# Kernel optimization log

Hardware: AMD Instinct MI355X
Metric: run time of the kernel (lower is better)

The kernel has to match this reference:

```python
import jax, jax.numpy as jnp
import numpy as np

# Routing structure from the torch module
GT0 = [[0,1,0,0,1,0],[0,1,0,0,0,1],[0,0,1,0,1,0],[0,0,1,0,0,1],[0,0,0,1,1,0],[0,0,0,1,0,1]]
NCLS = 6
K = 1  # top-k

def _expert_pairs():
    # For class i, expert index m = 1+(j-1)*5+(k-1) maps to atom1[j-1] -> atom2[k-1].
    pairs = []
    for i in range(NCLS):
        p = [(j - 1, k - 1) for j in range(1, 6) for k in range(1, 6)
             if j != k and GT0[i][j] == 1 and GT0[i][k] == 1]
        pairs.append(p)
    return pairs

PAIRS = _expert_pairs()  # each class has exactly 2 (atom1, atom2) pairs

B, P, D, H = 64, 256, 768, 3072

def setup_inputs() -> dict:
    key = jax.random.key(0)
    ks = jax.random.split(key, 8)
    s = 0.02
    x = jax.random.normal(ks[0], (B, NCLS + P, D), dtype=jnp.float32)
    mids = jax.random.randint(ks[1], (B,), 0, 6)
    moe0_W1 = jax.random.normal(ks[2], (D, H), dtype=jnp.float32) * s
    moe0_b1 = jnp.zeros((H,), jnp.float32)
    moe0_W2 = jax.random.normal(ks[3], (H, D), dtype=jnp.float32) * s
    moe0_b2 = jnp.zeros((D,), jnp.float32)
    A1_W = jax.random.normal(ks[4], (5, D, H), dtype=jnp.float32) * s  # atom1 linears
    A1_b = jnp.zeros((5, H), jnp.float32)
    A2_W = jax.random.normal(ks[5], (5, H, D), dtype=jnp.float32) * s  # atom2 linears
    A2_b = jnp.zeros((5, D), jnp.float32)
    G_W = jax.random.normal(ks[6], (NCLS, D, 2), dtype=jnp.float32) * s  # per-class gates (2 experts each, no bias)
    return {"x": x, "moe0_W1": moe0_W1, "moe0_b1": moe0_b1, "moe0_W2": moe0_W2,
            "moe0_b2": moe0_b2, "A1_W": A1_W, "A1_b": A1_b, "A2_W": A2_W,
            "A2_b": A2_b, "G_W": G_W, "mids": mids}

def _gelu(t):
    return jax.nn.gelu(t, approximate=False)  # torch nn.GELU default = erf

def reference(x, moe0_W1, moe0_b1, moe0_W2, moe0_b2, A1_W, A1_b, A2_W, A2_b, G_W, mids):
    cls_tokens = x[:, :NCLS]          # [B, 6, D]
    patch_tokens = x[:, NCLS:]        # [B, P, D]
    patch_out = _gelu(patch_tokens @ moe0_W1 + moe0_b1) @ moe0_W2 + moe0_b2  # [B, P, D]
    cls_outs = []
    for i in range(NCLS):
        tok = cls_tokens[:, i]        # [B, D]
        eouts = [ _gelu(tok @ A1_W[a] + A1_b[a]) @ A2_W[c] + A2_b[c] for (a, c) in PAIRS[i] ]
        out = jnp.stack(eouts, axis=-1)                 # [B, D, E=2]
        gate = jax.nn.softmax(tok @ G_W[i], axis=-1)    # [B, E]
        # top-k masking (k=1 < E=2): keep gates strictly above the (k+1)-th largest
        thr = jnp.sort(gate, axis=-1)[..., -(K + 1)]    # [B]
        mask = (gate > thr[..., None]).astype(gate.dtype)
        g = gate * mask
        g = g / jnp.clip(jnp.sum(g, axis=-1, keepdims=True), 1e-6)
        cls_outs.append(jnp.sum(out * g[:, None, :], axis=-1))  # [B, D]
    cls_out = jnp.stack(cls_outs, axis=1)               # [B, 6, D]
    return jnp.concatenate([cls_out, patch_out], axis=1)  # [B, 6+P, D]
```

## Files before the change

### kernel.cpp

```cpp
#include <hip/hip_runtime.h>
#include <hip/hip_bf16.h>

#define DD 768
#define HH 3072
#define BB 64
#define TT 262

typedef __bf16 bf16x8 __attribute__((ext_vector_type(8)));
typedef float f32x4 __attribute__((ext_vector_type(4)));
typedef unsigned short u16;
typedef unsigned int u32;

__device__ __constant__ int A_FIRST[12]  = {0,3, 0,4, 1,3, 1,4, 2,3, 2,4};
__device__ __constant__ int A_SECOND[12] = {3,0, 4,0, 3,1, 4,1, 3,2, 4,2};

__device__ __forceinline__ float gelu_f(float x) {
  float n2t = x * fmaf(x * x, -0.0713548163f, -1.5957691216f);
  return x * __builtin_amdgcn_rcpf(1.0f + __expf(n2t));
}

__device__ __forceinline__ u16 f2bf(float x) {
  u32 u = __builtin_bit_cast(u32, x);
  return (u16)((u + 0x7fffu + ((u >> 16) & 1u)) >> 16);
}

__device__ __forceinline__ void load_lds16(const void* g, void* l) {
  __builtin_amdgcn_global_load_lds(
      (const __attribute__((address_space(1))) void*)g,
      (__attribute__((address_space(3))) void*)l,
      16, 0, 0);
}

#define VMCNT(n) asm volatile("s_waitcnt vmcnt(" #n ")")
#define BAR() __builtin_amdgcn_s_barrier()

__global__ __launch_bounds__(256)
void preproc(const float* __restrict__ x,
             const float* __restrict__ W1, const float* __restrict__ A1W,
             const float* __restrict__ W2, const float* __restrict__ A2W,
             const float* __restrict__ GW,
             __hip_bfloat16* __restrict__ xb,
             __hip_bfloat16* __restrict__ W1t, __hip_bfloat16* __restrict__ A1t,
             __hip_bfloat16* __restrict__ W2t, __hip_bfloat16* __restrict__ A2t,
             int* __restrict__ sel) {
  __shared__ __hip_bfloat16 tile[32][33];
  const int bx = blockIdx.x;
  const int tid = threadIdx.x;
  if (bx < 12576) {
    int i = bx * 256 + tid;
    float4 v = ((const float4*)x)[i];
    union { u16 s[4]; uint2 d; } pk;
    pk.s[0] = f2bf(v.x); pk.s[1] = f2bf(v.y); pk.s[2] = f2bf(v.z); pk.s[3] = f2bf(v.w);
    *(uint2*)((u16*)xb + (size_t)i * 4) = pk.d;
  } else if (bx < 40224) {
    int R, C;
    const float* ip;
    __hip_bfloat16* op;
    int t;
    if (bx < 26400) {
      t = bx - 12576; R = DD; C = HH;
      int z = t / 2304; t %= 2304;
      ip = z ? (A1W + (size_t)(z - 1) * DD * HH) : W1;
      op = z ? (A1t + (size_t)(z - 1) * DD * HH) : W1t;
    } else {
      t = bx - 26400; R = HH; C = DD;
      int z = t / 2304; t %= 2304;
      ip = z ? (A2W + (size_t)(z - 1) * DD * HH) : W2;
      op = z ? (A2t + (size_t)(z - 1) * DD * HH) : W2t;
    }
    int ctiles = C >> 5;
    int c0 = (t % ctiles) * 32, r0 = (t / ctiles) * 32;
    int tx = tid & 31, ty = tid >> 5;
#pragma unroll
    for (int s = 0; s < 4; ++s) {
      int rr = ty * 4 + s;
      tile[rr][tx] = __float2bfloat16(ip[(size_t)(r0 + rr) * C + c0 + tx]);
    }
    __syncthreads();
#pragma unroll
    for (int s = 0; s < 4; ++s) {
      int cc = ty * 4 + s;
      op[(size_t)(c0 + cc) * R + r0 + tx] = tile[tx][cc];
    }
  } else {
    int unit = (bx - 40224) * 4 + (tid >> 6);
    int lane = tid & 63;
    int b = unit & 63, i = unit >> 6;
    const float* tok = x + (size_t)(b * TT + i) * DD;
    const float* g = GW + (size_t)i * DD * 2;
    float p0 = 0.f, p1 = 0.f;
    for (int k = lane; k < DD; k += 64) {
      float tv = tok[k];
      p0 += tv * g[k * 2 + 0];
      p1 += tv * g[k * 2 + 1];
    }
#pragma unroll
    for (int o = 32; o; o >>= 1) { p0 += __shfl_xor(p0, o); p1 += __shfl_xor(p1, o); }
    if (lane == 0) sel[i * 64 + b] = (p0 > p1) ? 0 : ((p1 > p0) ? 1 : 2);
  }
}

template <int MH, int KS>
__device__ __forceinline__ void rd_a(bf16x8 (&af)[4], const char* ab, int a_rd0) {
#pragma unroll
  for (int ii = 0; ii < 4; ++ii)
    af[ii] = *(const bf16x8*)(ab + MH * 16384 + ii * 2048 + (a_rd0 ^ (KS << 6)));
}
template <int KS>
__device__ __forceinline__ void rd_b(bf16x8 (&bf)[4], const char* bb, int b_rd0) {
#pragma unroll
  for (int j = 0; j < 4; ++j)
    bf[j] = *(const bf16x8*)(bb + (j >> 1) * 16384 + (j & 1) * 2048 + (b_rd0 ^ (KS << 6)));
}
template <int MH>
__device__ __forceinline__ void mma16(f32x4 (&acc)[8][4], const bf16x8 (&af)[4], const bf16x8 (&bf)[4]) {
  __builtin_amdgcn_s_setprio(1);
#pragma unroll
  for (int ii = 0; ii < 4; ++ii)
#pragma unroll
    for (int j = 0; j < 4; ++j)
      acc[MH * 4 + ii][j] =
          __builtin_amdgcn_mfma_f32_16x16x32_bf16(bf[j], af[ii], acc[MH * 4 + ii][j], 0, 0, 0);
  __builtin_amdgcn_s_setprio(0);
}

template <int MODE>
__device__ __forceinline__
void gemm_big(char* __restrict__ smem, int bx,
              const __hip_bfloat16* __restrict__ A,
              const __hip_bfloat16* __restrict__ Bw,
              const float* __restrict__ bias,
              void* __restrict__ Out) {
  constexpr int KDIM = (MODE == 0) ? DD : HH;
  constexpr int KT = KDIM / 64;
  constexpr int KB = KDIM * 2;

  char* As = smem;
  char* Bs = smem + 65536;

  const int tid = threadIdx.x;
  const int lane = tid & 63;
  const int q = lane >> 4;
  const int r = lane & 15;
  const int wave = tid >> 6;
  const int wave_m = wave >> 2;
  const int wave_n = wave & 3;

  int m0, n0;
  if constexpr (MODE == 0) {
    int chunk = bx / 192, local = bx % 192;
    m0 = (chunk * 16 + local % 16) * 256;
    n0 = (local / 16) * 256;
  } else {
    m0 = (bx % 64) * 256;
    n0 = (bx / 64) * 256;
  }

  const int trow = tid >> 3;
  const int sw = ((tid & 7) ^ (trow & 7)) << 4;
  size_t a_row;
  if constexpr (MODE == 0) a_row = (size_t)((m0 >> 8) * TT + 6 + trow);
  else                     a_row = (size_t)(m0 + trow);
  const char* gA = (const char*)A + a_row * KB + sw;
  const char* gB = (const char*)Bw + (size_t)(n0 + trow) * KB + sw;
  const int ldsb = (tid & ~63) * 16;

#define STAGE_A(h, kt, bsel) do { \
    load_lds16(gA + (size_t)((h) * 128) * KB + (kt) * 128,      As + ((bsel) << 15) + (h) * 16384 + ldsb); \
    load_lds16(gA + (size_t)((h) * 128 + 64) * KB + (kt) * 128, As + ((bsel) << 15) + (h) * 16384 + 8192 + ldsb); \
  } while (0)
#define STAGE_B(h, kt, bsel) do { \
    load_lds16(gB + (size_t)((h) * 128) * KB + (kt) * 128,      Bs + ((bsel) << 15) + (h) * 16384 + ldsb); \
    load_lds16(gB + (size_t)((h) * 128 + 64) * KB + (kt) * 128, Bs + ((bsel) << 15) + (h) * 16384 + 8192 + ldsb); \
  } while (0)

  const int a_rd0 = (wave_m * 64 + r) * 128 + ((q ^ (r & 7)) << 4);
  const int b_rd0 = (wave_n * 32 + r) * 128 + ((q ^ (r & 7)) << 4);

  f32x4 acc[8][4];
#pragma unroll
  for (int i = 0; i < 8; ++i)
#pragma unroll
    for (int j = 0; j < 4; ++j) acc[i][j] = (f32x4){0.f, 0.f, 0.f, 0.f};
  bf16x8 af[4], bf0[4], bf1[4];

  STAGE_A(0, 0, 0); STAGE_B(0, 0, 0); STAGE_B(1, 0, 0); STAGE_A(1, 0, 0);
  VMCNT(2);
  BAR();

  for (int t = 0; t < KT - 1; ++t) {
    const int bsel = t & 1, nsel = bsel ^ 1;
    const char* ab = As + (bsel << 15);
    const char* bb = Bs + (bsel << 15);
    rd_a<0, 0>(af, ab, a_rd0);
    rd_b<0>(bf0, bb, b_rd0);
    STAGE_A(0, t + 1, nsel);
    BAR();
    mma16<0>(acc, af, bf0);
    BAR();
    rd_a<0, 1>(af, ab, a_rd0);
    rd_b<1>(bf1, bb, b_rd0);
    STAGE_B(0, t + 1, nsel);
    BAR();
    mma16<0>(acc, af, bf1);
    VMCNT(4);
    BAR();
    rd_a<1, 0>(af, ab, a_rd0);
    STAGE_B(1, t + 1, nsel);
    BAR();
    mma16<1>(acc, af, bf0);
    BAR();
    rd_a<1, 1>(af, ab, a_rd0);
    STAGE_A(1, t + 1, nsel);
    BAR();
    mma16<1>(acc, af, bf1);
    VMCNT(2);
    BAR();
  }
  {
    const char* ab = As + (((KT - 1) & 1) << 15);
    const char* bb = Bs + (((KT - 1) & 1) << 15);
    rd_a<0, 0>(af, ab, a_rd0);
    rd_b<0>(bf0, bb, b_rd0);
    BAR(); mma16<0>(acc, af, bf0); BAR();
    rd_a<0, 1>(af, ab, a_rd0);
    rd_b<1>(bf1, bb, b_rd0);
    BAR(); mma16<0>(acc, af, bf1);
    VMCNT(0);
    BAR();
    rd_a<1, 0>(af, ab, a_rd0);
    BAR(); mma16<1>(acc, af, bf0); BAR();
    rd_a<1, 1>(af, ab, a_rd0);
    BAR(); mma16<1>(acc, af, bf1);
  }
#undef STAGE_A
#undef STAGE_B

#pragma unroll
  for (int i = 0; i < 8; ++i) {
    const int m_g = m0 + (i >> 2) * 128 + wave_m * 64 + (i & 3) * 16 + r;
#pragma unroll
    for (int j = 0; j < 4; ++j) {
      const int n_g = n0 + (j >> 1) * 128 + wave_n * 32 + (j & 1) * 16 + q * 4;
      f32x4 v = acc[i][j];
      v += *(const f32x4*)(bias + n_g);
      if constexpr (MODE == 0) {
        union { u16 s[4]; uint2 d; } pk;
#pragma unroll
        for (int rg = 0; rg < 4; ++rg) pk.s[rg] = f2bf(gelu_f(v[rg]));
        *(uint2*)((u16*)Out + (size_t)m_g * HH + n_g) = pk.d;
      } else {
        const int b = m_g >> 8, p = m_g & 255;
        *(f32x4*)((float*)Out + (size_t)(b * TT + 6 + p) * DD + n_g) = v;
      }
    }
  }
}

template <int MODE>
__device__ __forceinline__
void gemm_cls(char* __restrict__ smem, int bx,
              const __hip_bfloat16* __restrict__ A,
              const __hip_bfloat16* __restrict__ Bw,
              const float* __restrict__ bias,
              void* __restrict__ Out, const int* __restrict__ sel) {
  constexpr int KDIM = (MODE == 2) ? DD : HH;
  constexpr int KT = KDIM / 64;
  char* As = smem;
  char* Bs = smem + 8192;

  const int tid = threadIdx.x;
  const int lane = tid & 63;
  const int q = lane >> 4;
  const int r = lane & 15;
  const int wave = tid >> 6;
  const int wave_m = wave >> 2;
  const int wave_n = wave & 3;

  int n0, combo, e;
  if constexpr (MODE == 2) { n0 = (bx % 24) * 128; combo = bx / 24; e = A_FIRST[combo]; }
  else                     { n0 = (bx % 6) * 128;  combo = bx / 6;  e = A_SECOND[combo]; }
  const int cls_i = combo >> 1;
  const __hip_bfloat16* Bp = Bw + (size_t)e * DD * HH;
  const float* biasp = bias + e * ((MODE == 2) ? HH : DD);

  const int trow = tid >> 3;
  const int sw = ((tid & 7) ^ (trow & 7)) << 4;
  const char* gA = (const char*)A +
      ((MODE == 2) ? (size_t)(trow * TT + cls_i) * (DD * 2)
                   : (size_t)(combo * 64 + trow) * (HH * 2)) + sw;
  const char* gB = (const char*)Bp + (size_t)(n0 + trow) * (KDIM * 2) + sw;
  const int ldsb = (tid & ~63) * 16;
  const int sa = (q ^ (r & 7)) << 4;

  f32x4 acc[2][2];
  acc[0][0] = acc[0][1] = acc[1][0] = acc[1][1] = (f32x4){0.f, 0.f, 0.f, 0.f};

  for (int t = 0; t < KT; ++t) {
    load_lds16(gA + t * 128, As + ldsb);
    load_lds16(gB + t * 128, Bs + ldsb);
    load_lds16(gB + (size_t)64 * (KDIM * 2) + t * 128, Bs + 8192 + ldsb);
    __syncthreads();
#pragma unroll
    for (int ks = 0; ks < 2; ++ks) {
      bf16x8 a0 = *(const bf16x8*)(As + (wave_m * 32 + r) * 128 + (sa ^ (ks << 6)));
      bf16x8 a1 = *(const bf16x8*)(As + (wave_m * 32 + 16 + r) * 128 + (sa ^ (ks << 6)));
      bf16x8 b0 = *(const bf16x8*)(Bs + (wave_n * 32 + r) * 128 + (sa ^ (ks << 6)));
      bf16x8 b1 = *(const bf16x8*)(Bs + (wave_n * 32 + 16 + r) * 128 + (sa ^ (ks << 6)));
      acc[0][0] = __builtin_amdgcn_mfma_f32_16x16x32_bf16(b0, a0, acc[0][0], 0, 0, 0);
      acc[0][1] = __builtin_amdgcn_mfma_f32_16x16x32_bf16(b1, a0, acc[0][1], 0, 0, 0);
      acc[1][0] = __builtin_amdgcn_mfma_f32_16x16x32_bf16(b0, a1, acc[1][0], 0, 0, 0);
      acc[1][1] = __builtin_amdgcn_mfma_f32_16x16x32_bf16(b1, a1, acc[1][1], 0, 0, 0);
    }
    __syncthreads();
  }

#pragma unroll
  for (int i = 0; i < 2; ++i) {
    const int m_g = wave_m * 32 + i * 16 + r;
#pragma unroll
    for (int j = 0; j < 2; ++j) {
      const int n_g = n0 + wave_n * 32 + j * 16 + q * 4;
      f32x4 v = acc[i][j];
      v += *(const f32x4*)(biasp + n_g);
      if constexpr (MODE == 2) {
        union { u16 s[4]; uint2 d; } pk;
#pragma unroll
        for (int rg = 0; rg < 4; ++rg) pk.s[rg] = f2bf(gelu_f(v[rg]));
        *(uint2*)((u16*)Out + (size_t)(combo * 64 + m_g) * HH + n_g) = pk.d;
      } else {
        const int s = sel[cls_i * 64 + m_g];
        const int jj = combo & 1;
        float* dst = (float*)Out + (size_t)(m_g * TT + cls_i) * DD + n_g;
        if (s == jj)                    *(f32x4*)dst = v;
        else if (jj == 0 && s == 2)     *(f32x4*)dst = (f32x4){0.f, 0.f, 0.f, 0.f};
      }
    }
  }
}

__global__ __launch_bounds__(512, 2)
void mega1(const __hip_bfloat16* __restrict__ xb, const __hip_bfloat16* __restrict__ W1t,
           const float* __restrict__ b1, __hip_bfloat16* __restrict__ hid,
           const __hip_bfloat16* __restrict__ A1t, const float* __restrict__ A1b,
           __hip_bfloat16* __restrict__ hcls) {
  __shared__ __align__(16) char smem[131072];
  int bx = blockIdx.x;
  if (bx < 768) gemm_big<0>(smem, bx, xb, W1t, b1, hid);
  else          gemm_cls<2>(smem, bx - 768, xb, A1t, A1b, hcls, nullptr);
}

__global__ __launch_bounds__(512, 2)
void mega2(const __hip_bfloat16* __restrict__ hid, const __hip_bfloat16* __restrict__ W2t,
           const float* __restrict__ b2, float* __restrict__ out,
           const __hip_bfloat16* __restrict__ hcls, const __hip_bfloat16* __restrict__ A2t,
           const float* __restrict__ A2b, const int* __restrict__ sel) {
  __shared__ __align__(16) char smem[131072];
  int bx = blockIdx.x;
  if (bx < 192) gemm_big<1>(smem, bx, hid, W2t, b2, out);
  else          gemm_cls<3>(smem, bx - 192, hcls, A2t, A2b, out, sel);
}

extern "C" void kernel_launch(void* const* d_in, const int* in_sizes, int n_in,
                              void* d_out, int out_size, void* d_ws, size_t ws_size,
                              hipStream_t stream) {
  const float* x   = (const float*)d_in[0];
  const float* W1  = (const float*)d_in[1];
  const float* b1  = (const float*)d_in[2];
  const float* W2  = (const float*)d_in[3];
  const float* b2  = (const float*)d_in[4];
  const float* A1W = (const float*)d_in[5];
  const float* A1b = (const float*)d_in[6];
  const float* A2W = (const float*)d_in[7];
  const float* A2b = (const float*)d_in[8];
  const float* GW  = (const float*)d_in[9];
  float* out = (float*)d_out;

  char* ws = (char*)d_ws;
  __hip_bfloat16* xb   = (__hip_bfloat16*)(ws + 0);
  __hip_bfloat16* W1t  = (__hip_bfloat16*)(ws + 25755648);
  __hip_bfloat16* W2t  = (__hip_bfloat16*)(ws + 30474240);
  __hip_bfloat16* A1t  = (__hip_bfloat16*)(ws + 35192832);
  __hip_bfloat16* A2t  = (__hip_bfloat16*)(ws + 58785792);
  __hip_bfloat16* hcls = (__hip_bfloat16*)(ws + 82378752);
  int* sel             = (int*)(ws + 87097344);
  __hip_bfloat16* hid  = (__hip_bfloat16*)(ws + 87099136);

  preproc<<<40320, 256, 0, stream>>>(x, W1, A1W, W2, A2W, GW, xb, W1t, A1t, W2t, A2t, sel);
  mega1<<<1056, 512, 0, stream>>>(xb, W1t, b1, hid, A1t, A1b, hcls);
  mega2<<<264, 512, 0, stream>>>(hid, W2t, b2, out, hcls, A2t, A2b, sel);
}
```

Baseline: 398.6 us.

## Split LDS into named half-tile arrays and unroll GEMM K-loop by two

The single 128KB shared buffer is replaced by eight separately named 16KB arrays, so the compiler can see that the LDS regions are disjoint and schedule reads and async loads more freely. The big GEMM main loop is unrolled two K-tiles per iteration, with the stage buffers swapped statically and the vmcnt waits retuned to the new issue order. The prologue now prefetches more of the next tile. The cls GEMM is adapted to the split B halves. Risks are a longer code body and possible mis-ordering if the new wait counts are wrong.

```diff
diff --git a/kernel.cpp b/kernel.cpp
--- a/kernel.cpp
+++ b/kernel.cpp
@@ -31,7 +31,7 @@
       16, 0, 0);
 }
 
-#define VMCNT(n) asm volatile("s_waitcnt vmcnt(" #n ")")
+#define VMCNT(n) asm volatile("s_waitcnt vmcnt(" #n ")" ::: "memory")
 #define BAR() __builtin_amdgcn_s_barrier()
 
 __global__ __launch_bounds__(256)
@@ -100,18 +100,24 @@
   }
 }
 
-template <int MH, int KS>
-__device__ __forceinline__ void rd_a(bf16x8 (&af)[4], const char* ab, int a_rd0) {
+__device__ __forceinline__ void rd_a4(bf16x8 (&af)[4], const char (&arr)[16384], int base) {
 #pragma unroll
   for (int ii = 0; ii < 4; ++ii)
-    af[ii] = *(const bf16x8*)(ab + MH * 16384 + ii * 2048 + (a_rd0 ^ (KS << 6)));
-}
-template <int KS>
-__device__ __forceinline__ void rd_b(bf16x8 (&bf)[4], const char* bb, int b_rd0) {
-#pragma unroll
-  for (int j = 0; j < 4; ++j)
-    bf[j] = *(const bf16x8*)(bb + (j >> 1) * 16384 + (j & 1) * 2048 + (b_rd0 ^ (KS << 6)));
-}
+    af[ii] = *(const bf16x8*)(&arr[base + ii * 2048]);
+}
+__device__ __forceinline__ void rd_b4(bf16x8 (&bf)[4], const char (&L)[16384],
+                                      const char (&H)[16384], int base) {
+#pragma unroll
+  for (int j = 0; j < 2; ++j) {
+    bf[j]     = *(const bf16x8*)(&L[base + j * 2048]);
+    bf[2 + j] = *(const bf16x8*)(&H[base + j * 2048]);
+  }
+}
+__device__ __forceinline__ void st2(const char* g, size_t rs, char (&arr)[16384], int ldsb) {
+  load_lds16(g,      &arr[ldsb]);
+  load_lds16(g + rs, &arr[8192 + ldsb]);
+}
+
 template <int MH>
 __device__ __forceinline__ void mma16(f32x4 (&acc)[8][4], const bf16x8 (&af)[4], const bf16x8 (&bf)[4]) {
   __builtin_amdgcn_s_setprio(1);
@@ -126,25 +132,22 @@
 
 template <int MODE>
 __device__ __forceinline__
-void gemm_big(char* __restrict__ smem, int bx,
-              const __hip_bfloat16* __restrict__ A,
-              const __hip_bfloat16* __restrict__ Bw,
-              const float* __restrict__ bias,
-              void* __restrict__ Out) {
+void gemm_big(int bx,
+              char (&A0s0)[16384], char (&A1s0)[16384], char (&B0s0)[16384], char (&B1s0)[16384],
+              char (&A0s1)[16384], char (&A1s1)[16384], char (&B0s1)[16384], char (&B1s1)[16384],
+              const __hip_bfloat16* __restrict__ A, const __hip_bfloat16* __restrict__ Bw,
+              const float* __restrict__ bias, void* __restrict__ Out) {
   constexpr int KDIM = (MODE == 0) ? DD : HH;
   constexpr int KT = KDIM / 64;
-  constexpr int KB = KDIM * 2;
-
-  char* As = smem;
-  char* Bs = smem + 65536;
+  constexpr int ITER = KT / 2;
+  constexpr size_t KB = (size_t)KDIM * 2;
+  constexpr size_t R64 = 64 * KB, R128 = 128 * KB;
 
   const int tid = threadIdx.x;
   const int lane = tid & 63;
-  const int q = lane >> 4;
-  const int r = lane & 15;
+  const int q = lane >> 4, r = lane & 15;
   const int wave = tid >> 6;
-  const int wave_m = wave >> 2;
-  const int wave_n = wave & 3;
+  const int wave_m = wave >> 2, wave_n = wave & 3;
 
   int m0, n0;
   if constexpr (MODE == 0) {
@@ -165,15 +168,6 @@
   const char* gB = (const char*)Bw + (size_t)(n0 + trow) * KB + sw;
   const int ldsb = (tid & ~63) * 16;
 
-#define STAGE_A(h, kt, bsel) do { \
-    load_lds16(gA + (size_t)((h) * 128) * KB + (kt) * 128,      As + ((bsel) << 15) + (h) * 16384 + ldsb); \
-    load_lds16(gA + (size_t)((h) * 128 + 64) * KB + (kt) * 128, As + ((bsel) << 15) + (h) * 16384 + 8192 + ldsb); \
-  } while (0)
-#define STAGE_B(h, kt, bsel) do { \
-    load_lds16(gB + (size_t)((h) * 128) * KB + (kt) * 128,      Bs + ((bsel) << 15) + (h) * 16384 + ldsb); \
-    load_lds16(gB + (size_t)((h) * 128 + 64) * KB + (kt) * 128, Bs + ((bsel) << 15) + (h) * 16384 + 8192 + ldsb); \
-  } while (0)
-
   const int a_rd0 = (wave_m * 64 + r) * 128 + ((q ^ (r & 7)) << 4);
   const int b_rd0 = (wave_n * 32 + r) * 128 + ((q ^ (r & 7)) << 4);
 
@@ -184,57 +178,69 @@
     for (int j = 0; j < 4; ++j) acc[i][j] = (f32x4){0.f, 0.f, 0.f, 0.f};
   bf16x8 af[4], bf0[4], bf1[4];
 
-  STAGE_A(0, 0, 0); STAGE_B(0, 0, 0); STAGE_B(1, 0, 0); STAGE_A(1, 0, 0);
-  VMCNT(2);
+  st2(gA,          R64, A0s0, ldsb);
+  st2(gB,          R64, B0s0, ldsb);
+  st2(gB + R128,   R64, B1s0, ldsb);
+  st2(gA + R128,   R64, A1s0, ldsb);
+  st2(gA + 128,    R64, A0s1, ldsb);
+  st2(gB + 128,    R64, B0s1, ldsb);
+  VMCNT(6);
   BAR();
 
-  for (int t = 0; t < KT - 1; ++t) {
-    const int bsel = t & 1, nsel = bsel ^ 1;
-    const char* ab = As + (bsel << 15);
-    const char* bb = Bs + (bsel << 15);
-    rd_a<0, 0>(af, ab, a_rd0);
-    rd_b<0>(bf0, bb, b_rd0);
-    STAGE_A(0, t + 1, nsel);
-    BAR();
-    mma16<0>(acc, af, bf0);
-    BAR();
-    rd_a<0, 1>(af, ab, a_rd0);
-    rd_b<1>(bf1, bb, b_rd0);
-    STAGE_B(0, t + 1, nsel);
-    BAR();
-    mma16<0>(acc, af, bf1);
-    VMCNT(4);
-    BAR();
-    rd_a<1, 0>(af, ab, a_rd0);
-    STAGE_B(1, t + 1, nsel);
-    BAR();
-    mma16<1>(acc, af, bf0);
-    BAR();
-    rd_a<1, 1>(af, ab, a_rd0);
-    STAGE_A(1, t + 1, nsel);
-    BAR();
-    mma16<1>(acc, af, bf1);
-    VMCNT(2);
-    BAR();
-  }
-  {
-    const char* ab = As + (((KT - 1) & 1) << 15);
-    const char* bb = Bs + (((KT - 1) & 1) << 15);
-    rd_a<0, 0>(af, ab, a_rd0);
-    rd_b<0>(bf0, bb, b_rd0);
+  for (int i = 0; i < ITER - 1; ++i) {
+    rd_a4(af, A0s0, a_rd0);
+    rd_b4(bf0, B0s0, B1s0, b_rd0);
+    st2(gB + R128 + 128, R64, B1s1, ldsb);
     BAR(); mma16<0>(acc, af, bf0); BAR();
-    rd_a<0, 1>(af, ab, a_rd0);
-    rd_b<1>(bf1, bb, b_rd0);
-    BAR(); mma16<0>(acc, af, bf1);
-    VMCNT(0);
-    BAR();
-    rd_a<1, 0>(af, ab, a_rd0);
+    rd_a4(af, A0s0, a_rd0 ^ 64);
+    rd_b4(bf1, B0s0, B1s0, b_rd0 ^ 64);
+    st2(gA + R128 + 128, R64, A1s1, ldsb);
+    BAR(); mma16<0>(acc, af, bf1); VMCNT(8); BAR();
+    rd_a4(af, A1s0, a_rd0);
+    st2(gA + 256, R64, A0s0, ldsb);
     BAR(); mma16<1>(acc, af, bf0); BAR();
-    rd_a<1, 1>(af, ab, a_rd0);
-    BAR(); mma16<1>(acc, af, bf1);
-  }
-#undef STAGE_A
-#undef STAGE_B
+    rd_a4(af, A1s0, a_rd0 ^ 64);
+    st2(gB + 256, R64, B0s0, ldsb);
+    BAR(); mma16<1>(acc, af, bf1); VMCNT(6); BAR();
+    rd_a4(af, A0s1, a_rd0);
+    rd_b4(bf0, B0s1, B1s1, b_rd0);
+    st2(gB + R128 + 256, R64, B1s0, ldsb);
+    BAR(); mma16<0>(acc, af, bf0); BAR();
+    rd_a4(af, A0s1, a_rd0 ^ 64);
+    rd_b4(bf1, B0s1, B1s1, b_rd0 ^ 64);
+    st2(gA + R128 + 256, R64, A1s0, ldsb);
+    BAR(); mma16<0>(acc, af, bf1); VMCNT(8); BAR();
+    rd_a4(af, A1s1, a_rd0);
+    st2(gA + 384, R64, A0s1, ldsb);
+    BAR(); mma16<1>(acc, af, bf0); BAR();
+    rd_a4(af, A1s1, a_rd0 ^ 64);
+    st2(gB + 384, R64, B0s1, ldsb);
+    BAR(); mma16<1>(acc, af, bf1); VMCNT(6); BAR();
+    gA += 256; gB += 256;
+  }
+
+  rd_a4(af, A0s0, a_rd0);
+  rd_b4(bf0, B0s0, B1s0, b_rd0);
+  st2(gB + R128 + 128, R64, B1s1, ldsb);
+  BAR(); mma16<0>(acc, af, bf0); BAR();
+  rd_a4(af, A0s0, a_rd0 ^ 64);
+  rd_b4(bf1, B0s0, B1s0, b_rd0 ^ 64);
+  st2(gA + R128 + 128, R64, A1s1, ldsb);
+  BAR(); mma16<0>(acc, af, bf1); VMCNT(8); BAR();
+  rd_a4(af, A1s0, a_rd0);
+  BAR(); mma16<1>(acc, af, bf0); BAR();
+  rd_a4(af, A1s0, a_rd0 ^ 64);
+  BAR(); mma16<1>(acc, af, bf1); VMCNT(2); BAR();
+  rd_a4(af, A0s1, a_rd0);
+  rd_b4(bf0, B0s1, B1s1, b_rd0);
+  BAR(); mma16<0>(acc, af, bf0); BAR();
+  rd_a4(af, A0s1, a_rd0 ^ 64);
+  rd_b4(bf1, B0s1, B1s1, b_rd0 ^ 64);
+  BAR(); mma16<0>(acc, af, bf1); VMCNT(0); BAR();
+  rd_a4(af, A1s1, a_rd0);
+  BAR(); mma16<1>(acc, af, bf0); BAR();
+  rd_a4(af, A1s1, a_rd0 ^ 64);
+  BAR(); mma16<1>(acc, af, bf1);
 
 #pragma unroll
   for (int i = 0; i < 8; ++i) {
@@ -259,23 +265,17 @@
 
 template <int MODE>
 __device__ __forceinline__
-void gemm_cls(char* __restrict__ smem, int bx,
-              const __hip_bfloat16* __restrict__ A,
-              const __hip_bfloat16* __restrict__ Bw,
-              const float* __restrict__ bias,
-              void* __restrict__ Out, const int* __restrict__ sel) {
+void gemm_cls(int bx, char (&Asp)[16384], char (&BsL)[16384], char (&BsH)[16384],
+              const __hip_bfloat16* __restrict__ A, const __hip_bfloat16* __restrict__ Bw,
+              const float* __restrict__ bias, void* __restrict__ Out, const int* __restrict__ sel) {
   constexpr int KDIM = (MODE == 2) ? DD : HH;
   constexpr int KT = KDIM / 64;
-  char* As = smem;
-  char* Bs = smem + 8192;
 
   const int tid = threadIdx.x;
   const int lane = tid & 63;
-  const int q = lane >> 4;
-  const int r = lane & 15;
+  const int q = lane >> 4, r = lane & 15;
   const int wave = tid >> 6;
-  const int wave_m = wave >> 2;
-  const int wave_n = wave & 3;
+  const int wave_m = wave >> 2, wave_n = wave & 3;
 
   int n0, combo, e;
   if constexpr (MODE == 2) { n0 = (bx % 24) * 128; combo = bx / 24; e = A_FIRST[combo]; }
@@ -296,17 +296,20 @@
   f32x4 acc[2][2];
   acc[0][0] = acc[0][1] = acc[1][0] = acc[1][1] = (f32x4){0.f, 0.f, 0.f, 0.f};
 
+  const char* bb = (wave_n < 2) ? &BsL[0] : &BsH[0];
+  const int brow = (wave_n & 1) * 32;
+
   for (int t = 0; t < KT; ++t) {
-    load_lds16(gA + t * 128, As + ldsb);
-    load_lds16(gB + t * 128, Bs + ldsb);
-    load_lds16(gB + (size_t)64 * (KDIM * 2) + t * 128, Bs + 8192 + ldsb);
+    load_lds16(gA + t * 128, &Asp[ldsb]);
+    load_lds16(gB + t * 128, &BsL[ldsb]);
+    load_lds16(gB + (size_t)64 * (KDIM * 2) + t * 128, &BsH[ldsb]);
     __syncthreads();
 #pragma unroll
     for (int ks = 0; ks < 2; ++ks) {
-      bf16x8 a0 = *(const bf16x8*)(As + (wave_m * 32 + r) * 128 + (sa ^ (ks << 6)));
-      bf16x8 a1 = *(const bf16x8*)(As + (wave_m * 32 + 16 + r) * 128 + (sa ^ (ks << 6)));
-      bf16x8 b0 = *(const bf16x8*)(Bs + (wave_n * 32 + r) * 128 + (sa ^ (ks << 6)));
-      bf16x8 b1 = *(const bf16x8*)(Bs + (wave_n * 32 + 16 + r) * 128 + (sa ^ (ks << 6)));
+      bf16x8 a0 = *(const bf16x8*)(&Asp[(wave_m * 32 + r) * 128 + (sa ^ (ks << 6))]);
+      bf16x8 a1 = *(const bf16x8*)(&Asp[(wave_m * 32 + 16 + r) * 128 + (sa ^ (ks << 6))]);
+      bf16x8 b0 = *(const bf16x8*)(bb + (brow + r) * 128 + (sa ^ (ks << 6)));
+      bf16x8 b1 = *(const bf16x8*)(bb + (brow + 16 + r) * 128 + (sa ^ (ks << 6)));
       acc[0][0] = __builtin_amdgcn_mfma_f32_16x16x32_bf16(b0, a0, acc[0][0], 0, 0, 0);
       acc[0][1] = __builtin_amdgcn_mfma_f32_16x16x32_bf16(b1, a0, acc[0][1], 0, 0, 0);
       acc[1][0] = __builtin_amdgcn_mfma_f32_16x16x32_bf16(b0, a1, acc[1][0], 0, 0, 0);
@@ -344,10 +347,11 @@
            const float* __restrict__ b1, __hip_bfloat16* __restrict__ hid,
            const __hip_bfloat16* __restrict__ A1t, const float* __restrict__ A1b,
            __hip_bfloat16* __restrict__ hcls) {
-  __shared__ __align__(16) char smem[131072];
+  __shared__ __align__(16) char A0s0[16384], A1s0[16384], B0s0[16384], B1s0[16384],
+                                A0s1[16384], A1s1[16384], B0s1[16384], B1s1[16384];
   int bx = blockIdx.x;
-  if (bx < 768) gemm_big<0>(smem, bx, xb, W1t, b1, hid);
-  else          gemm_cls<2>(smem, bx - 768, xb, A1t, A1b, hcls, nullptr);
+  if (bx < 768) gemm_big<0>(bx, A0s0, A1s0, B0s0, B1s0, A0s1, A1s1, B0s1, B1s1, xb, W1t, b1, hid);
+  else          gemm_cls<2>(bx - 768, A0s0, B0s0, B1s0, xb, A1t, A1b, hcls, nullptr);
 }
 
 __global__ __launch_bounds__(512, 2)
@@ -355,10 +359,11 @@
            const float* __restrict__ b2, float* __restrict__ out,
            const __hip_bfloat16* __restrict__ hcls, const __hip_bfloat16* __restrict__ A2t,
            const float* __restrict__ A2b, const int* __restrict__ sel) {
-  __shared__ __align__(16) char smem[131072];
+  __shared__ __align__(16) char A0s0[16384], A1s0[16384], B0s0[16384], B1s0[16384],
+                                A0s1[16384], A1s1[16384], B0s1[16384], B1s1[16384];
   int bx = blockIdx.x;
-  if (bx < 192) gemm_big<1>(smem, bx, hid, W2t, b2, out);
-  else          gemm_cls<3>(smem, bx - 192, hcls, A2t, A2b, out, sel);
+  if (bx < 192) gemm_big<1>(bx, A0s0, A1s0, B0s0, B1s0, A0s1, A1s1, B0s1, B1s1, hid, W2t, b2, out);
+  else          gemm_cls<3>(bx - 192, A0s0, B0s0, B1s0, hcls, A2t, A2b, out, sel);
 }
 
 extern "C" void kernel_launch(void* const* d_in, const int* in_sizes, int n_in,
```

New measurement: 419.4 us. +5.2%, slower.

## Unroll big GEMM main loop by two k-tiles with deeper prefetch and inline-asm LDS reads

Applied to the files above, without the earlier changes.

Rewrites the large-GEMM main loop to process two k-tiles per iteration. Global-to-LDS staging is issued further ahead, with six quarter-tiles in flight at the prologue and vmcnt waits adjusted to match. LDS fragment reads now go through inline-asm ds_read_b128 with immediate offsets and explicit lgkmcnt waits plus sched barriers, meant to cut address arithmetic and give tighter control over MFMA/load interleaving. In exchange, manual waitcnt handling is fragile, and the sched barriers may block compiler scheduling.

```diff
diff --git a/kernel.cpp b/kernel.cpp
--- a/kernel.cpp
+++ b/kernel.cpp
@@ -33,6 +33,14 @@
 
 #define VMCNT(n) asm volatile("s_waitcnt vmcnt(" #n ")")
 #define BAR() __builtin_amdgcn_s_barrier()
+#define WAIT_FRAGS() do { asm volatile("s_waitcnt lgkmcnt(0)"); __builtin_amdgcn_sched_barrier(0); } while (0)
+
+template <int IMM>
+__device__ __forceinline__ bf16x8 dsr(u32 addr) {
+  f32x4 o;
+  asm volatile("ds_read_b128 %0, %1 offset:%c2" : "=v"(o) : "v"(addr), "i"(IMM));
+  return __builtin_bit_cast(bf16x8, o);
+}
 
 __global__ __launch_bounds__(256)
 void preproc(const float* __restrict__ x,
@@ -100,18 +108,22 @@
   }
 }
 
-template <int MH, int KS>
-__device__ __forceinline__ void rd_a(bf16x8 (&af)[4], const char* ab, int a_rd0) {
-#pragma unroll
-  for (int ii = 0; ii < 4; ++ii)
-    af[ii] = *(const bf16x8*)(ab + MH * 16384 + ii * 2048 + (a_rd0 ^ (KS << 6)));
-}
-template <int KS>
-__device__ __forceinline__ void rd_b(bf16x8 (&bf)[4], const char* bb, int b_rd0) {
-#pragma unroll
-  for (int j = 0; j < 4; ++j)
-    bf[j] = *(const bf16x8*)(bb + (j >> 1) * 16384 + (j & 1) * 2048 + (b_rd0 ^ (KS << 6)));
-}
+template <int R>
+__device__ __forceinline__ void rdA4(bf16x8 (&af)[4], u32 a) {
+  af[0] = dsr<R + 0>(a);    af[1] = dsr<R + 2048>(a);
+  af[2] = dsr<R + 4096>(a); af[3] = dsr<R + 6144>(a);
+}
+template <int R>
+__device__ __forceinline__ void rdB4(bf16x8 (&bf)[4], u32 b) {
+  bf[0] = dsr<R + 0>(b);     bf[1] = dsr<R + 2048>(b);
+  bf[2] = dsr<R + 16384>(b); bf[3] = dsr<R + 18432>(b);
+}
+
+__device__ __forceinline__ void st2r(const char* g, size_t r64, char* smem, int region, int ldsb) {
+  load_lds16(g,       smem + region + ldsb);
+  load_lds16(g + r64, smem + region + 8192 + ldsb);
+}
+
 template <int MH>
 __device__ __forceinline__ void mma16(f32x4 (&acc)[8][4], const bf16x8 (&af)[4], const bf16x8 (&bf)[4]) {
   __builtin_amdgcn_s_setprio(1);
@@ -127,24 +139,21 @@
 template <int MODE>
 __device__ __forceinline__
 void gemm_big(char* __restrict__ smem, int bx,
-              const __hip_bfloat16* __restrict__ A,
-              const __hip_bfloat16* __restrict__ Bw,
-              const float* __restrict__ bias,
-              void* __restrict__ Out) {
+              const __hip_bfloat16* __restrict__ A, const __hip_bfloat16* __restrict__ Bw,
+              const float* __restrict__ bias, void* __restrict__ Out) {
   constexpr int KDIM = (MODE == 0) ? DD : HH;
   constexpr int KT = KDIM / 64;
-  constexpr int KB = KDIM * 2;
-
-  char* As = smem;
-  char* Bs = smem + 65536;
+  constexpr int ITER = KT / 2;
+  constexpr size_t KB = (size_t)KDIM * 2;
+  constexpr size_t R64 = 64 * KB, R128 = 128 * KB;
+  constexpr int A0S0 = 0, A1S0 = 16384, A0S1 = 32768, A1S1 = 49152;
+  constexpr int BB0S0 = 65536, BB1S0 = 81920, BB0S1 = 98304, BB1S1 = 114688;
 
   const int tid = threadIdx.x;
   const int lane = tid & 63;
-  const int q = lane >> 4;
-  const int r = lane & 15;
+  const int q = lane >> 4, r = lane & 15;
   const int wave = tid >> 6;
-  const int wave_m = wave >> 2;
-  const int wave_n = wave & 3;
+  const int wave_m = wave >> 2, wave_n = wave & 3;
 
   int m0, n0;
   if constexpr (MODE == 0) {
@@ -165,17 +174,11 @@
   const char* gB = (const char*)Bw + (size_t)(n0 + trow) * KB + sw;
   const int ldsb = (tid & ~63) * 16;
 
-#define STAGE_A(h, kt, bsel) do { \
-    load_lds16(gA + (size_t)((h) * 128) * KB + (kt) * 128,      As + ((bsel) << 15) + (h) * 16384 + ldsb); \
-    load_lds16(gA + (size_t)((h) * 128 + 64) * KB + (kt) * 128, As + ((bsel) << 15) + (h) * 16384 + 8192 + ldsb); \
-  } while (0)
-#define STAGE_B(h, kt, bsel) do { \
-    load_lds16(gB + (size_t)((h) * 128) * KB + (kt) * 128,      Bs + ((bsel) << 15) + (h) * 16384 + ldsb); \
-    load_lds16(gB + (size_t)((h) * 128 + 64) * KB + (kt) * 128, Bs + ((bsel) << 15) + (h) * 16384 + 8192 + ldsb); \
-  } while (0)
-
-  const int a_rd0 = (wave_m * 64 + r) * 128 + ((q ^ (r & 7)) << 4);
-  const int b_rd0 = (wave_n * 32 + r) * 128 + ((q ^ (r & 7)) << 4);
+  const u32 lds0 = (u32)(uintptr_t)smem;
+  const u32 aA0 = lds0 + (wave_m * 64 + r) * 128 + ((q ^ (r & 7)) << 4);
+  const u32 aA1 = aA0 ^ 64;
+  const u32 aB0 = lds0 + 65536 + (wave_n * 32 + r) * 128 + ((q ^ (r & 7)) << 4);
+  const u32 aB1 = aB0 ^ 64;
 
   f32x4 acc[8][4];
 #pragma unroll
@@ -184,57 +187,70 @@
     for (int j = 0; j < 4; ++j) acc[i][j] = (f32x4){0.f, 0.f, 0.f, 0.f};
   bf16x8 af[4], bf0[4], bf1[4];
 
-  STAGE_A(0, 0, 0); STAGE_B(0, 0, 0); STAGE_B(1, 0, 0); STAGE_A(1, 0, 0);
-  VMCNT(2);
+  st2r(gA,        R64, smem, A0S0,  ldsb);
+  st2r(gB,        R64, smem, BB0S0, ldsb);
+  st2r(gB + R128, R64, smem, BB1S0, ldsb);
+  st2r(gA + R128, R64, smem, A1S0,  ldsb);
+  st2r(gA + 128,  R64, smem, A0S1,  ldsb);
+  st2r(gB + 128,  R64, smem, BB0S1, ldsb);
+  VMCNT(6);
   BAR();
 
-  for (int t = 0; t < KT - 1; ++t) {
-    const int bsel = t & 1, nsel = bsel ^ 1;
-    const char* ab = As + (bsel << 15);
-    const char* bb = Bs + (bsel << 15);
-    rd_a<0, 0>(af, ab, a_rd0);
-    rd_b<0>(bf0, bb, b_rd0);
-    STAGE_A(0, t + 1, nsel);
-    BAR();
-    mma16<0>(acc, af, bf0);
-    BAR();
-    rd_a<0, 1>(af, ab, a_rd0);
-    rd_b<1>(bf1, bb, b_rd0);
-    STAGE_B(0, t + 1, nsel);
-    BAR();
-    mma16<0>(acc, af, bf1);
-    VMCNT(4);
-    BAR();
-    rd_a<1, 0>(af, ab, a_rd0);
-    STAGE_B(1, t + 1, nsel);
-    BAR();
-    mma16<1>(acc, af, bf0);
-    BAR();
-    rd_a<1, 1>(af, ab, a_rd0);
-    STAGE_A(1, t + 1, nsel);
-    BAR();
-    mma16<1>(acc, af, bf1);
-    VMCNT(2);
-    BAR();
-  }
-  {
-    const char* ab = As + (((KT - 1) & 1) << 15);
-    const char* bb = Bs + (((KT - 1) & 1) << 15);
-    rd_a<0, 0>(af, ab, a_rd0);
-    rd_b<0>(bf0, bb, b_rd0);
-    BAR(); mma16<0>(acc, af, bf0); BAR();
-    rd_a<0, 1>(af, ab, a_rd0);
-    rd_b<1>(bf1, bb, b_rd0);
-    BAR(); mma16<0>(acc, af, bf1);
-    VMCNT(0);
-    BAR();
-    rd_a<1, 0>(af, ab, a_rd0);
-    BAR(); mma16<1>(acc, af, bf0); BAR();
-    rd_a<1, 1>(af, ab, a_rd0);
-    BAR(); mma16<1>(acc, af, bf1);
-  }
-#undef STAGE_A
-#undef STAGE_B
+#pragma unroll 1
+  for (int i = 0; i < ITER - 1; ++i) {
+    rdA4<A0S0>(af, aA0);
+    rdB4<0>(bf0, aB0);
+    st2r(gB + R128 + 128, R64, smem, BB1S1, ldsb);
+    BAR(); WAIT_FRAGS(); mma16<0>(acc, af, bf0); BAR();
+    rdA4<A0S0>(af, aA1);
+    rdB4<0>(bf1, aB1);
+    st2r(gA + R128 + 128, R64, smem, A1S1, ldsb);
+    BAR(); WAIT_FRAGS(); mma16<0>(acc, af, bf1); VMCNT(8); BAR();
+    rdA4<A1S0>(af, aA0);
+    st2r(gA + 256, R64, smem, A0S0, ldsb);
+    BAR(); WAIT_FRAGS(); mma16<1>(acc, af, bf0); BAR();
+    rdA4<A1S0>(af, aA1);
+    st2r(gB + 256, R64, smem, BB0S0, ldsb);
+    BAR(); WAIT_FRAGS(); mma16<1>(acc, af, bf1); VMCNT(6); BAR();
+    rdA4<A0S1>(af, aA0);
+    rdB4<32768>(bf0, aB0);
+    st2r(gB + R128 + 256, R64, smem, BB1S0, ldsb);
+    BAR(); WAIT_FRAGS(); mma16<0>(acc, af, bf0); BAR();
+    rdA4<A0S1>(af, aA1);
+    rdB4<32768>(bf1, aB1);
+    st2r(gA + R128 + 256, R64, smem, A1S0, ldsb);
+    BAR(); WAIT_FRAGS(); mma16<0>(acc, af, bf1); VMCNT(8); BAR();
+    rdA4<A1S1>(af, aA0);
+    st2r(gA + 384, R64, smem, A0S1, ldsb);
+    BAR(); WAIT_FRAGS(); mma16<1>(acc, af, bf0); BAR();
+    rdA4<A1S1>(af, aA1);
+    st2r(gB + 384, R64, smem, BB0S1, ldsb);
+    BAR(); WAIT_FRAGS(); mma16<1>(acc, af, bf1); VMCNT(6); BAR();
+    gA += 256; gB += 256;
+  }
+
+  rdA4<A0S0>(af, aA0);
+  rdB4<0>(bf0, aB0);
+  st2r(gB + R128 + 128, R64, smem, BB1S1, ldsb);
+  BAR(); WAIT_FRAGS(); mma16<0>(acc, af, bf0); BAR();
+  rdA4<A0S0>(af, aA1);
+  rdB4<0>(bf1, aB1);
+  st2r(gA + R128 + 128, R64, smem, A1S1, ldsb);
+  BAR(); WAIT_FRAGS(); mma16<0>(acc, af, bf1); VMCNT(8); BAR();
+  rdA4<A1S0>(af, aA0);
+  BAR(); WAIT_FRAGS(); mma16<1>(acc, af, bf0); BAR();
+  rdA4<A1S0>(af, aA1);
+  BAR(); WAIT_FRAGS(); mma16<1>(acc, af, bf1); VMCNT(2); BAR();
+  rdA4<A0S1>(af, aA0);
+  rdB4<32768>(bf0, aB0);
+  BAR(); WAIT_FRAGS(); mma16<0>(acc, af, bf0); BAR();
+  rdA4<A0S1>(af, aA1);
+  rdB4<32768>(bf1, aB1);
+  BAR(); WAIT_FRAGS(); mma16<0>(acc, af, bf1); VMCNT(0); BAR();
+  rdA4<A1S1>(af, aA0);
+  BAR(); WAIT_FRAGS(); mma16<1>(acc, af, bf0); BAR();
+  rdA4<A1S1>(af, aA1);
+  BAR(); WAIT_FRAGS(); mma16<1>(acc, af, bf1);
 
 #pragma unroll
   for (int i = 0; i < 8; ++i) {
@@ -260,10 +276,8 @@
 template <int MODE>
 __device__ __forceinline__
 void gemm_cls(char* __restrict__ smem, int bx,
-              const __hip_bfloat16* __restrict__ A,
-              const __hip_bfloat16* __restrict__ Bw,
-              const float* __restrict__ bias,
-              void* __restrict__ Out, const int* __restrict__ sel) {
+              const __hip_bfloat16* __restrict__ A, const __hip_bfloat16* __restrict__ Bw,
+              const float* __restrict__ bias, void* __restrict__ Out, const int* __restrict__ sel) {
   constexpr int KDIM = (MODE == 2) ? DD : HH;
   constexpr int KT = KDIM / 64;
   char* As = smem;
@@ -271,11 +285,9 @@
 
   const int tid = threadIdx.x;
   const int lane = tid & 63;
-  const int q = lane >> 4;
-  const int r = lane & 15;
+  const int q = lane >> 4, r = lane & 15;
   const int wave = tid >> 6;
-  const int wave_m = wave >> 2;
-  const int wave_n = wave & 3;
+  const int wave_m = wave >> 2, wave_n = wave & 3;
 
   int n0, combo, e;
   if constexpr (MODE == 2) { n0 = (bx % 24) * 128; combo = bx / 24; e = A_FIRST[combo]; }
```

Measured after the change: 387.2 us. 1.03x faster.
